# Kernel optimization log

Hardware: AMD Instinct MI355X
Metric: run time of the kernel (lower is better)

Reference implementation:

```python
import jax, jax.numpy as jnp
import numpy as np

B, L, D, H, S = 2, 2048, 1024, 16, 4
Dh = D // H
EPS = 1e-5


def setup_inputs() -> dict:
    key = jax.random.key(0)
    ks = jax.random.split(key, 12)
    sc = 0.02
    w = lambda k, shape: (jax.random.normal(k, shape, jnp.float32) * sc)
    M = 2 * S  # number of MHA blocks / dense linears
    inp = {
        "response": jax.random.normal(ks[0], (B, L, D), jnp.float32),
        "mask": jnp.broadcast_to(jnp.tril(jnp.ones((L, L), bool)), (B, L, L)),
        "Wq": w(ks[1], (M, D, D)), "bq": w(ks[2], (M, D)),
        "Wk": w(ks[3], (M, D, D)), "bk": w(ks[4], (M, D)),
        "Wv": w(ks[5], (M, D, D)), "bv": w(ks[6], (M, D)),
        "Wo": w(ks[7], (M, D, D)), "bo": w(ks[8], (M, D)),
        "Wd": w(ks[9], (M, D, D)), "bd": w(ks[10], (M, D)),
    }
    return inp


def _ln(x):
    # fresh LayerNorm(d) with default weight=1, bias=0, eps=1e-5
    m = jnp.mean(x, axis=-1, keepdims=True)
    v = jnp.mean((x - m) ** 2, axis=-1, keepdims=True)
    return (x - m) * jax.lax.rsqrt(v + EPS)


def _linear(x, W, b):
    # torch Linear: x @ W.T + b
    return jnp.einsum('bld,od->blo', x, W) + b


def _mha(x, i, mask, Wq, bq, Wk, bk, Wv, bv, Wo, bo):
    # self-attention: q = k = v = x
    split = lambda y: y.reshape(B, L, H, Dh).transpose(0, 2, 1, 3)  # (B,H,L,Dh)
    q = split(_linear(x, Wq[i], bq[i]))
    k = split(_linear(x, Wk[i], bk[i]))
    v = split(_linear(x, Wv[i], bv[i]))
    scores = jnp.einsum('bhqd,bhkd->bhqk', q, k) / jnp.sqrt(jnp.float32(Dh))
    if mask is not None:
        scores = jnp.where(mask[:, None, :, :], scores, -jnp.inf)
    p = jnp.nan_to_num(jax.nn.softmax(scores, axis=-1))
    o = jnp.einsum('bhqk,bhkd->bhqd', p, v).transpose(0, 2, 1, 3).reshape(B, L, D)
    return _linear(o, Wo[i], bo[i])


def reference(response, mask, Wq, bq, Wk, bk, Wv, bv, Wo, bo, Wd, bd):
    x = response
    for i in range(S):
        # masked self-attention + residual + LN
        x = _ln(x + _mha(x, 2 * i, mask, Wq, bq, Wk, bk, Wv, bv, Wo, bo))
        # encoder-attention sublayer (encMem is None -> unmasked self-attention)
        x = _ln(x + _mha(x, 2 * i + 1, None, Wq, bq, Wk, bk, Wv, bv, Wo, bo))
        # dense: linear[2i](LeakyReLU(linear[2i+1](x)))
        h = jax.nn.leaky_relu(_linear(x, Wd[2 * i + 1], bd[2 * i + 1]), negative_slope=0.01)
        h = _linear(h, Wd[2 * i], bd[2 * i])
        x = _ln(x + h)
    return x
```

## Files before the change

kernel.cpp:

```cpp
#include <hip/hip_runtime.h>
#include <stdint.h>
#include <stddef.h>

typedef __attribute__((ext_vector_type(8))) _Float16 f16x8;
typedef __attribute__((ext_vector_type(4))) _Float16 f16x4;
typedef __attribute__((ext_vector_type(4))) float    f32x4;

#define NB 2
#define NL 2048
#define ND 1024
#define NH 16
#define NROWS (NB*NL)

__device__ __forceinline__ void async16(void* lds, const void* g) {
  __builtin_amdgcn_global_load_lds(
      (const __attribute__((address_space(1))) void*)g,
      (__attribute__((address_space(3))) void*)lds, 16, 0, 0);
}

struct CvtArgs { const float* in[5]; _Float16* out[5]; };

__global__ __launch_bounds__(256) void cvt_all(CvtArgs a, int n4)
{
  const float* in  = a.in[blockIdx.z];
  _Float16*   out  = a.out[blockIdx.z];
  for (int i = blockIdx.x * blockDim.x + threadIdx.x; i < n4;
       i += gridDim.x * blockDim.x) {
    float4 v = ((const float4*)in)[i];
    f16x4 o = {(_Float16)v.x, (_Float16)v.y, (_Float16)v.z, (_Float16)v.w};
    ((f16x4*)out)[i] = o;
  }
}

__global__ __launch_bounds__(256) void init_x(
    const float* __restrict__ r, float* __restrict__ x,
    _Float16* __restrict__ xh, int n4)
{
  for (int i = blockIdx.x * blockDim.x + threadIdx.x; i < n4;
       i += gridDim.x * blockDim.x) {
    float4 v = ((const float4*)r)[i];
    ((float4*)x)[i] = v;
    f16x4 o = {(_Float16)v.x, (_Float16)v.y, (_Float16)v.z, (_Float16)v.w};
    ((f16x4*)xh)[i] = o;
  }
}

struct GArgs {
  const _Float16* A;
  const _Float16* B[3];
  const float*    bias[3];
  void*           out[3];
  int             mode[3];
  int             ksplit;
};

__global__ __launch_bounds__(256, 2) void gemm_bt(GArgs ga)
{
  __shared__ _Float16 As[2][128 * 64];
  __shared__ _Float16 Bs[2][128 * 64];
  const int tid = threadIdx.x;
  const int w = tid >> 6, l = tid & 63;
  const int ql = l & 15, g = l >> 4;
  const int z = blockIdx.z;
  const int widx = ga.ksplit ? 0 : (blockIdx.x >> 3);
  const _Float16* Bw  = ga.B[widx];
  const float*   bias = ga.bias[widx];
  void*          outp = ga.ksplit ? ga.out[z] : ga.out[widx];
  const int      mode = ga.mode[widx];
  const int kbeg = ga.ksplit ? z * (ND / 2) : 0;
  const int kend = ga.ksplit ? kbeg + ND / 2 : ND;
  const bool dobias = (!ga.ksplit) || (z == 0);
  const int brow = blockIdx.y * 128;
  const int bcol = (blockIdx.x & 7) * 128;
  const int wm = w >> 1, wn = w & 1;
  f32x4 acc[4][4] = {};

  const int srow = w * 32 + (l >> 3);
  const int scol = ((l & 7) ^ (l >> 3)) << 3;
  const _Float16* Ag = ga.A + (size_t)(brow + srow) * ND + scol;
  const _Float16* Bg = Bw   + (size_t)(bcol + srow) * ND + scol;

#define STAGE(buf, k0_)                                                  \
  {                                                                      \
    _Float16* AsW = &As[buf][w * 2048];                                  \
    _Float16* BsW = &Bs[buf][w * 2048];                                  \
    _Pragma("unroll")                                                    \
    for (int i = 0; i < 4; ++i) {                                        \
      async16(AsW + i * 512, Ag + (size_t)i * 8 * ND + (k0_));           \
      async16(BsW + i * 512, Bg + (size_t)i * 8 * ND + (k0_));           \
    }                                                                    \
  }

  STAGE(0, kbeg);
  for (int k0 = kbeg; k0 < kend; k0 += 64) {
    const int cur = ((k0 - kbeg) >> 6) & 1;
    if (k0 + 64 < kend) {
      STAGE(cur ^ 1, k0 + 64);
      asm volatile("s_waitcnt vmcnt(8)" ::: "memory");
    } else {
      asm volatile("s_waitcnt vmcnt(0)" ::: "memory");
    }
    __builtin_amdgcn_s_barrier();
#pragma unroll
    for (int ks = 0; ks < 64; ks += 32) {
      const int cx = (ks + g * 8) ^ ((ql & 7) << 3);
      f16x8 af[4], bf[4];
#pragma unroll
      for (int mi = 0; mi < 4; ++mi)
        af[mi] = *(const f16x8*)&As[cur][(wm * 64 + mi * 16 + ql) * 64 + cx];
#pragma unroll
      for (int nj = 0; nj < 4; ++nj)
        bf[nj] = *(const f16x8*)&Bs[cur][(wn * 64 + nj * 16 + ql) * 64 + cx];
#pragma unroll
      for (int mi = 0; mi < 4; ++mi)
#pragma unroll
        for (int nj = 0; nj < 4; ++nj)
          acc[mi][nj] = __builtin_amdgcn_mfma_f32_16x16x32_f16(
              af[mi], bf[nj], acc[mi][nj], 0, 0, 0);
    }
    asm volatile("s_waitcnt lgkmcnt(0)" ::: "memory");
    __builtin_amdgcn_s_barrier();
  }
#undef STAGE

  const int colb = bcol + wn * 64;
  const int rowb = brow + wm * 64 + g * 4;
  if (mode == 3) {
    _Float16* vt = (_Float16*)outp;
    const int bb = rowb >> 11;
#pragma unroll
    for (int nj = 0; nj < 4; ++nj) {
      const int col = colb + nj * 16 + ql;
      const float bv = bias[col];
      const int hh = col >> 6, d = col & 63;
      _Float16* vrow = vt + ((size_t)((bb * NH + hh) * 64 + d)) * NL;
#pragma unroll
      for (int mi = 0; mi < 4; ++mi) {
        const int krow = (rowb + mi * 16) & (NL - 1);
        f16x4 o;
#pragma unroll
        for (int r = 0; r < 4; ++r) o[r] = (_Float16)(acc[mi][nj][r] + bv);
        *(f16x4*)(vrow + krow) = o;
      }
    }
  } else {
    _Float16* oh = (_Float16*)outp;
#pragma unroll
    for (int nj = 0; nj < 4; ++nj) {
      const int col = colb + nj * 16 + ql;
      const float bv = dobias ? bias[col] : 0.f;
#pragma unroll
      for (int mi = 0; mi < 4; ++mi) {
#pragma unroll
        for (int r = 0; r < 4; ++r) {
          float v = acc[mi][nj][r] + bv;
          if (mode == 2) v = v > 0.f ? v : 0.01f * v;
          oh[(size_t)(rowb + mi * 16 + r) * ND + col] = (_Float16)v;
        }
      }
    }
  }
}

template<bool CAUSAL>
__global__ __launch_bounds__(512, 4) void attn_fwd(
    const _Float16* __restrict__ Q, const _Float16* __restrict__ K,
    const _Float16* __restrict__ Vt, _Float16* __restrict__ O)
{
  __shared__ _Float16 kv[3][2][64 * 64];
  __shared__ unsigned int pls[8][8 * 34];
  const int tid = threadIdx.x;
  const int w = tid >> 6, l = tid & 63;
  const int ql = l & 15, g = l >> 4;
  const int h = blockIdx.y, b = blockIdx.z;
  const int qt = (CAUSAL && b) ? (NL / 128 - 1 - (int)blockIdx.x) : blockIdx.x;
  const int qrow = qt * 128 + w * 16 + ql;

  const _Float16* Qp = Q + (size_t)(b * NL + qrow) * ND + h * 64 + g * 8;
  const f16x8 bq0 = *(const f16x8*)Qp;
  const f16x8 bq1 = *(const f16x8*)(Qp + 32);

  const int srow = w * 8 + (l >> 3);
  const int scol = ((l & 7) ^ (l >> 3)) << 3;
  const _Float16* Kg = K  + ((size_t)(b * NL) + srow) * ND + h * 64 + scol;
  const _Float16* Vg = Vt + ((size_t)((b * NH + h) * 64 + srow)) * NL + scol;

  const int msk  = (ql & 7) << 3;
  const int offA = ql * 64 + ((     g * 8) ^ msk);
  const int offB = ql * 64 + ((32 + g * 8) ^ msk);

  unsigned int* pw = &pls[w][0];
  f32x4 ot[4] = {};
  float s_run = 0.f;
  const int ntiles = CAUSAL ? (qt * 2 + 2) : (NL / 64);
  const float SCL = 0.125f * 1.44269504089f;
  const float M2  = 4.0f * 1.44269504089f;

  async16(&kv[0][0][w * 512], Kg);
  async16(&kv[0][1][w * 512], Vg);

  int cbuf = 0, sbuf = 1;
  for (int kt = 0; kt < ntiles; ++kt) {
    const size_t nk0 = (size_t)((kt + 1 < ntiles) ? kt + 1 : kt) * 64;
    async16(&kv[sbuf][0][w * 512], Kg + nk0 * ND);
    async16(&kv[sbuf][1][w * 512], Vg + nk0);
    asm volatile("s_waitcnt vmcnt(2)" ::: "memory");
    __builtin_amdgcn_s_barrier();

    const _Float16* kb = &kv[cbuf][0][0];
    const _Float16* vb = &kv[cbuf][1][0];
    const int k0 = kt * 64;
    f32x4 st[4] = {};
#pragma unroll
    for (int sub = 0; sub < 4; ++sub) {
      const f16x8 a0 = *(const f16x8*)&kb[sub * 1024 + offA];
      const f16x8 a1 = *(const f16x8*)&kb[sub * 1024 + offB];
      st[sub] = __builtin_amdgcn_mfma_f32_16x16x32_f16(a0, bq0, st[sub], 0, 0, 0);
      st[sub] = __builtin_amdgcn_mfma_f32_16x16x32_f16(a1, bq1, st[sub], 0, 0, 0);
    }
    float ps = 0.f;
    float pv[16];
#pragma unroll
    for (int sub = 0; sub < 4; ++sub)
#pragma unroll
      for (int r = 0; r < 4; ++r) {
        float p = exp2f(__builtin_fmaf(st[sub][r], SCL, -M2));
        if (CAUSAL && (k0 + sub * 16 + g * 4 + r) > qrow) p = 0.f;
        pv[sub * 4 + r] = p;
        ps += p;
      }
    ps += __shfl_xor(ps, 16);
    ps += __shfl_xor(ps, 32);
    s_run += ps;

#pragma unroll
    for (int sub = 0; sub < 2; ++sub) {
      uint2 uu;
      uu.x = __builtin_bit_cast(unsigned int,
                __builtin_amdgcn_cvt_pkrtz(pv[sub * 4 + 0], pv[sub * 4 + 1]));
      uu.y = __builtin_bit_cast(unsigned int,
                __builtin_amdgcn_cvt_pkrtz(pv[sub * 4 + 2], pv[sub * 4 + 3]));
      *(uint2*)&pw[(sub * 4 + g) * 34 + 2 * ql] = uu;
    }
    {
      uint2 lo = *(const uint2*)&pw[(2 * g    ) * 34 + 2 * ql];
      uint2 hi = *(const uint2*)&pw[(2 * g + 1) * 34 + 2 * ql];
      uint4 ui; ui.x = lo.x; ui.y = lo.y; ui.z = hi.x; ui.w = hi.y;
      const f16x8 pf = __builtin_bit_cast(f16x8, ui);
#pragma unroll
      for (int dt = 0; dt < 4; ++dt) {
        const f16x8 vf = *(const f16x8*)&vb[dt * 1024 + offA];
        ot[dt] = __builtin_amdgcn_mfma_f32_16x16x32_f16(vf, pf, ot[dt], 0, 0, 0);
      }
    }
#pragma unroll
    for (int sub = 2; sub < 4; ++sub) {
      uint2 uu;
      uu.x = __builtin_bit_cast(unsigned int,
                __builtin_amdgcn_cvt_pkrtz(pv[sub * 4 + 0], pv[sub * 4 + 1]));
      uu.y = __builtin_bit_cast(unsigned int,
                __builtin_amdgcn_cvt_pkrtz(pv[sub * 4 + 2], pv[sub * 4 + 3]));
      *(uint2*)&pw[((sub - 2) * 4 + g) * 34 + 2 * ql] = uu;
    }
    {
      uint2 lo = *(const uint2*)&pw[(2 * g    ) * 34 + 2 * ql];
      uint2 hi = *(const uint2*)&pw[(2 * g + 1) * 34 + 2 * ql];
      uint4 ui; ui.x = lo.x; ui.y = lo.y; ui.z = hi.x; ui.w = hi.y;
      const f16x8 pf = __builtin_bit_cast(f16x8, ui);
#pragma unroll
      for (int dt = 0; dt < 4; ++dt) {
        const f16x8 vf = *(const f16x8*)&vb[dt * 1024 + offB];
        ot[dt] = __builtin_amdgcn_mfma_f32_16x16x32_f16(vf, pf, ot[dt], 0, 0, 0);
      }
    }
    cbuf = sbuf;
    sbuf = sbuf + 1 == 3 ? 0 : sbuf + 1;
  }

  const float inv = 1.f / s_run;
#pragma unroll
  for (int dt = 0; dt < 4; ++dt) {
    f16x4 o;
#pragma unroll
    for (int r = 0; r < 4; ++r) o[r] = (_Float16)(ot[dt][r] * inv);
    *(f16x4*)(O + (size_t)(b * NL + qrow) * ND + h * 64 + dt * 16 + g * 4) = o;
  }
}

__global__ __launch_bounds__(256) void resid_ln(
    const float* __restrict__ x, const _Float16* __restrict__ d0,
    const _Float16* __restrict__ d1,
    float* __restrict__ xo, _Float16* __restrict__ xh)
{
  const int row = blockIdx.x, tid = threadIdx.x;
  const float4 xv = ((const float4*)(x + (size_t)row * ND))[tid];
  const f16x4 v0 = ((const f16x4*)(d0 + (size_t)row * ND))[tid];
  const f16x4 v1 = ((const f16x4*)(d1 + (size_t)row * ND))[tid];
  const float a = xv.x + (float)v0[0] + (float)v1[0];
  const float b = xv.y + (float)v0[1] + (float)v1[1];
  const float c = xv.z + (float)v0[2] + (float)v1[2];
  const float d = xv.w + (float)v0[3] + (float)v1[3];
  float s = a + b + c + d;
  float ss = a * a + b * b + c * c + d * d;
#pragma unroll
  for (int m = 1; m < 64; m <<= 1) {
    s  += __shfl_xor(s, m);
    ss += __shfl_xor(ss, m);
  }
  __shared__ float red[8];
  if ((tid & 63) == 0) { red[tid >> 6] = s; red[4 + (tid >> 6)] = ss; }
  __syncthreads();
  const float S  = red[0] + red[1] + red[2] + red[3];
  const float SS = red[4] + red[5] + red[6] + red[7];
  const float mean = S * (1.0f / ND);
  const float var  = SS * (1.0f / ND) - mean * mean;
  const float rstd = rsqrtf(fmaxf(var, 0.f) + 1e-5f);
  float4 y;
  y.x = (a - mean) * rstd; y.y = (b - mean) * rstd;
  y.z = (c - mean) * rstd; y.w = (d - mean) * rstd;
  ((float4*)(xo + (size_t)row * ND))[tid] = y;
  f16x4 yh = {(_Float16)y.x, (_Float16)y.y, (_Float16)y.z, (_Float16)y.w};
  ((f16x4*)(xh + (size_t)row * ND))[tid] = yh;
}

extern "C" void kernel_launch(void* const* d_in, const int* in_sizes, int n_in,
                              void* d_out, int out_size, void* d_ws, size_t ws_size,
                              hipStream_t stream)
{
  (void)in_sizes; (void)n_in; (void)out_size; (void)ws_size;
  const float* response = (const float*)d_in[0];
  const float* Wq = (const float*)d_in[2];
  const float* bq = (const float*)d_in[3];
  const float* Wk = (const float*)d_in[4];
  const float* bk = (const float*)d_in[5];
  const float* Wv = (const float*)d_in[6];
  const float* bv = (const float*)d_in[7];
  const float* Wo = (const float*)d_in[8];
  const float* bo = (const float*)d_in[9];
  const float* Wd = (const float*)d_in[10];
  const float* bd = (const float*)d_in[11];
  float* x = (float*)d_out;

  const size_t MB = 1024 * 1024;
  char* p = (char*)d_ws;
  _Float16* Wq_h = (_Float16*)(p + 0 * MB);
  _Float16* Wk_h = (_Float16*)(p + 16 * MB);
  _Float16* Wv_h = (_Float16*)(p + 32 * MB);
  _Float16* Wo_h = (_Float16*)(p + 48 * MB);
  _Float16* Wd_h = (_Float16*)(p + 64 * MB);
  _Float16* xh   = (_Float16*)(p + 80 * MB);
  _Float16* Qh   = (_Float16*)(p + 88 * MB);
  _Float16* Kh   = (_Float16*)(p + 96 * MB);
  _Float16* Vth  = (_Float16*)(p + 104 * MB);
  _Float16* Oh   = (_Float16*)(p + 112 * MB);
  _Float16* h1   = Qh;
  _Float16* t0   = (_Float16*)(p + 96 * MB);
  _Float16* t1   = (_Float16*)(p + 104 * MB);

  const int wn4 = 8 * 1024 * 1024 / 4;
  CvtArgs ca = { { Wq, Wk, Wv, Wo, Wd }, { Wq_h, Wk_h, Wv_h, Wo_h, Wd_h } };
  cvt_all<<<dim3(256, 1, 5), 256, 0, stream>>>(ca, wn4);
  init_x<<<1024, 256, 0, stream>>>(response, x, xh, NROWS * ND / 4);

  const dim3 g3(24, NROWS / 128, 1);
  const dim3 gs(8, NROWS / 128, 2);
  const dim3 gf(8, NROWS / 128, 1);
  const dim3 agrid(NL / 128, NH, NB);

  for (int i = 0; i < 4; ++i) {
    for (int sub = 0; sub < 2; ++sub) {
      const int m = 2 * i + sub;
      const size_t wo = (size_t)m * MB;
      const size_t bf = (size_t)m * 1024;
      GArgs qkv = { xh,
                    { Wq_h + wo, Wk_h + wo, Wv_h + wo },
                    { bq + bf, bk + bf, bv + bf },
                    { Qh, Kh, Vth }, { 0, 0, 3 }, 0 };
      gemm_bt<<<g3, 256, 0, stream>>>(qkv);
      if (sub == 0) attn_fwd<true ><<<agrid, 512, 0, stream>>>(Qh, Kh, Vth, Oh);
      else          attn_fwd<false><<<agrid, 512, 0, stream>>>(Qh, Kh, Vth, Oh);
      GArgs oprj = { Oh,
                     { Wo_h + wo, nullptr, nullptr },
                     { bo + bf, nullptr, nullptr },
                     { t0, t1, nullptr }, { 0, 0, 0 }, 1 };
      gemm_bt<<<gs, 256, 0, stream>>>(oprj);
      resid_ln<<<NROWS, 256, 0, stream>>>(x, t0, t1, x, xh);
    }
    const size_t w1 = (size_t)(2 * i + 1) * MB, b1 = (size_t)(2 * i + 1) * 1024;
    const size_t w0 = (size_t)(2 * i) * MB,     b0 = (size_t)(2 * i) * 1024;
    GArgs f1 = { xh,
                 { Wd_h + w1, nullptr, nullptr },
                 { bd + b1, nullptr, nullptr },
                 { h1, nullptr, nullptr }, { 2, 0, 0 }, 0 };
    gemm_bt<<<gf, 256, 0, stream>>>(f1);
    GArgs f2 = { h1,
                 { Wd_h + w0, nullptr, nullptr },
                 { bd + b0, nullptr, nullptr },
                 { t0, t1, nullptr }, { 0, 0, 0 }, 1 };
    gemm_bt<<<gs, 256, 0, stream>>>(f2);
    resid_ln<<<NROWS, 256, 0, stream>>>(x, t0, t1, x, xh);
  }
}
```

Before: 1.237 ms.

## Keep residual stream in fp16, widen conversion stores, raise MFMA wave priority

Drops the fp32 copy of the residual stream: each residual+LayerNorm reads and writes only the fp16 activations, and fp32 output is written only in the final layer. The weight and input conversion kernels now emit 8-wide fp16 stores, and the weight conversion grid is larger. s_setprio is raised around the MFMA blocks in the GEMM and attention loops so matrix-heavy waves are favoured by the scheduler. The residual path loses precision by accumulating in fp16 across twelve sublayers.

```diff
diff --git a/kernel.cpp b/kernel.cpp
--- a/kernel.cpp
+++ b/kernel.cpp
@@ -20,28 +20,30 @@
 
 struct CvtArgs { const float* in[5]; _Float16* out[5]; };
 
-__global__ __launch_bounds__(256) void cvt_all(CvtArgs a, int n4)
+__global__ __launch_bounds__(256) void cvt_all(CvtArgs a, int n8)
 {
   const float* in  = a.in[blockIdx.z];
   _Float16*   out  = a.out[blockIdx.z];
-  for (int i = blockIdx.x * blockDim.x + threadIdx.x; i < n4;
+  for (int i = blockIdx.x * blockDim.x + threadIdx.x; i < n8;
        i += gridDim.x * blockDim.x) {
-    float4 v = ((const float4*)in)[i];
-    f16x4 o = {(_Float16)v.x, (_Float16)v.y, (_Float16)v.z, (_Float16)v.w};
-    ((f16x4*)out)[i] = o;
+    float4 v0 = ((const float4*)in)[2 * i];
+    float4 v1 = ((const float4*)in)[2 * i + 1];
+    f16x8 o = {(_Float16)v0.x, (_Float16)v0.y, (_Float16)v0.z, (_Float16)v0.w,
+               (_Float16)v1.x, (_Float16)v1.y, (_Float16)v1.z, (_Float16)v1.w};
+    ((f16x8*)out)[i] = o;
   }
 }
 
 __global__ __launch_bounds__(256) void init_x(
-    const float* __restrict__ r, float* __restrict__ x,
-    _Float16* __restrict__ xh, int n4)
-{
-  for (int i = blockIdx.x * blockDim.x + threadIdx.x; i < n4;
+    const float* __restrict__ r, _Float16* __restrict__ xh, int n8)
+{
+  for (int i = blockIdx.x * blockDim.x + threadIdx.x; i < n8;
        i += gridDim.x * blockDim.x) {
-    float4 v = ((const float4*)r)[i];
-    ((float4*)x)[i] = v;
-    f16x4 o = {(_Float16)v.x, (_Float16)v.y, (_Float16)v.z, (_Float16)v.w};
-    ((f16x4*)xh)[i] = o;
+    float4 v0 = ((const float4*)r)[2 * i];
+    float4 v1 = ((const float4*)r)[2 * i + 1];
+    f16x8 o = {(_Float16)v0.x, (_Float16)v0.y, (_Float16)v0.z, (_Float16)v0.w,
+               (_Float16)v1.x, (_Float16)v1.y, (_Float16)v1.z, (_Float16)v1.w};
+    ((f16x8*)xh)[i] = o;
   }
 }
 
@@ -101,6 +103,7 @@
       asm volatile("s_waitcnt vmcnt(0)" ::: "memory");
     }
     __builtin_amdgcn_s_barrier();
+    __builtin_amdgcn_s_setprio(1);
 #pragma unroll
     for (int ks = 0; ks < 64; ks += 32) {
       const int cx = (ks + g * 8) ^ ((ql & 7) << 3);
@@ -118,6 +121,7 @@
           acc[mi][nj] = __builtin_amdgcn_mfma_f32_16x16x32_f16(
               af[mi], bf[nj], acc[mi][nj], 0, 0, 0);
     }
+    __builtin_amdgcn_s_setprio(0);
     asm volatile("s_waitcnt lgkmcnt(0)" ::: "memory");
     __builtin_amdgcn_s_barrier();
   }
@@ -211,6 +215,7 @@
     const _Float16* vb = &kv[cbuf][1][0];
     const int k0 = kt * 64;
     f32x4 st[4] = {};
+    __builtin_amdgcn_s_setprio(1);
 #pragma unroll
     for (int sub = 0; sub < 4; ++sub) {
       const f16x8 a0 = *(const f16x8*)&kb[sub * 1024 + offA];
@@ -218,6 +223,7 @@
       st[sub] = __builtin_amdgcn_mfma_f32_16x16x32_f16(a0, bq0, st[sub], 0, 0, 0);
       st[sub] = __builtin_amdgcn_mfma_f32_16x16x32_f16(a1, bq1, st[sub], 0, 0, 0);
     }
+    __builtin_amdgcn_s_setprio(0);
     float ps = 0.f;
     float pv[16];
 #pragma unroll
@@ -247,11 +253,13 @@
       uint2 hi = *(const uint2*)&pw[(2 * g + 1) * 34 + 2 * ql];
       uint4 ui; ui.x = lo.x; ui.y = lo.y; ui.z = hi.x; ui.w = hi.y;
       const f16x8 pf = __builtin_bit_cast(f16x8, ui);
+      __builtin_amdgcn_s_setprio(1);
 #pragma unroll
       for (int dt = 0; dt < 4; ++dt) {
         const f16x8 vf = *(const f16x8*)&vb[dt * 1024 + offA];
         ot[dt] = __builtin_amdgcn_mfma_f32_16x16x32_f16(vf, pf, ot[dt], 0, 0, 0);
       }
+      __builtin_amdgcn_s_setprio(0);
     }
 #pragma unroll
     for (int sub = 2; sub < 4; ++sub) {
@@ -267,11 +275,13 @@
       uint2 hi = *(const uint2*)&pw[(2 * g + 1) * 34 + 2 * ql];
       uint4 ui; ui.x = lo.x; ui.y = lo.y; ui.z = hi.x; ui.w = hi.y;
       const f16x8 pf = __builtin_bit_cast(f16x8, ui);
+      __builtin_amdgcn_s_setprio(1);
 #pragma unroll
       for (int dt = 0; dt < 4; ++dt) {
         const f16x8 vf = *(const f16x8*)&vb[dt * 1024 + offB];
         ot[dt] = __builtin_amdgcn_mfma_f32_16x16x32_f16(vf, pf, ot[dt], 0, 0, 0);
       }
+      __builtin_amdgcn_s_setprio(0);
     }
     cbuf = sbuf;
     sbuf = sbuf + 1 == 3 ? 0 : sbuf + 1;
@@ -287,19 +297,20 @@
   }
 }
 
+template<bool FINAL>
 __global__ __launch_bounds__(256) void resid_ln(
-    const float* __restrict__ x, const _Float16* __restrict__ d0,
+    const _Float16* __restrict__ xh_in, const _Float16* __restrict__ d0,
     const _Float16* __restrict__ d1,
-    float* __restrict__ xo, _Float16* __restrict__ xh)
+    _Float16* __restrict__ xh_out, float* __restrict__ xf)
 {
   const int row = blockIdx.x, tid = threadIdx.x;
-  const float4 xv = ((const float4*)(x + (size_t)row * ND))[tid];
+  const f16x4 xv = ((const f16x4*)(xh_in + (size_t)row * ND))[tid];
   const f16x4 v0 = ((const f16x4*)(d0 + (size_t)row * ND))[tid];
   const f16x4 v1 = ((const f16x4*)(d1 + (size_t)row * ND))[tid];
-  const float a = xv.x + (float)v0[0] + (float)v1[0];
-  const float b = xv.y + (float)v0[1] + (float)v1[1];
-  const float c = xv.z + (float)v0[2] + (float)v1[2];
-  const float d = xv.w + (float)v0[3] + (float)v1[3];
+  const float a = (float)xv[0] + (float)v0[0] + (float)v1[0];
+  const float b = (float)xv[1] + (float)v0[1] + (float)v1[1];
+  const float c = (float)xv[2] + (float)v0[2] + (float)v1[2];
+  const float d = (float)xv[3] + (float)v0[3] + (float)v1[3];
   float s = a + b + c + d;
   float ss = a * a + b * b + c * c + d * d;
 #pragma unroll
@@ -315,12 +326,15 @@
   const float mean = S * (1.0f / ND);
   const float var  = SS * (1.0f / ND) - mean * mean;
   const float rstd = rsqrtf(fmaxf(var, 0.f) + 1e-5f);
-  float4 y;
-  y.x = (a - mean) * rstd; y.y = (b - mean) * rstd;
-  y.z = (c - mean) * rstd; y.w = (d - mean) * rstd;
-  ((float4*)(xo + (size_t)row * ND))[tid] = y;
-  f16x4 yh = {(_Float16)y.x, (_Float16)y.y, (_Float16)y.z, (_Float16)y.w};
-  ((f16x4*)(xh + (size_t)row * ND))[tid] = yh;
+  const float ya = (a - mean) * rstd, yb = (b - mean) * rstd;
+  const float yc = (c - mean) * rstd, yd = (d - mean) * rstd;
+  if (FINAL) {
+    float4 y; y.x = ya; y.y = yb; y.z = yc; y.w = yd;
+    ((float4*)(xf + (size_t)row * ND))[tid] = y;
+  } else {
+    f16x4 yh = {(_Float16)ya, (_Float16)yb, (_Float16)yc, (_Float16)yd};
+    ((f16x4*)(xh_out + (size_t)row * ND))[tid] = yh;
+  }
 }
 
 extern "C" void kernel_launch(void* const* d_in, const int* in_sizes, int n_in,
@@ -339,7 +353,7 @@
   const float* bo = (const float*)d_in[9];
   const float* Wd = (const float*)d_in[10];
   const float* bd = (const float*)d_in[11];
-  float* x = (float*)d_out;
+  float* xf = (float*)d_out;
 
   const size_t MB = 1024 * 1024;
   char* p = (char*)d_ws;
@@ -357,10 +371,10 @@
   _Float16* t0   = (_Float16*)(p + 96 * MB);
   _Float16* t1   = (_Float16*)(p + 104 * MB);
 
-  const int wn4 = 8 * 1024 * 1024 / 4;
+  const int wn8 = 8 * 1024 * 1024 / 8;
   CvtArgs ca = { { Wq, Wk, Wv, Wo, Wd }, { Wq_h, Wk_h, Wv_h, Wo_h, Wd_h } };
-  cvt_all<<<dim3(256, 1, 5), 256, 0, stream>>>(ca, wn4);
-  init_x<<<1024, 256, 0, stream>>>(response, x, xh, NROWS * ND / 4);
+  cvt_all<<<dim3(512, 1, 5), 256, 0, stream>>>(ca, wn8);
+  init_x<<<1024, 256, 0, stream>>>(response, xh, NROWS * ND / 8);
 
   const dim3 g3(24, NROWS / 128, 1);
   const dim3 gs(8, NROWS / 128, 2);
@@ -384,7 +398,7 @@
                      { bo + bf, nullptr, nullptr },
                      { t0, t1, nullptr }, { 0, 0, 0 }, 1 };
       gemm_bt<<<gs, 256, 0, stream>>>(oprj);
-      resid_ln<<<NROWS, 256, 0, stream>>>(x, t0, t1, x, xh);
+      resid_ln<false><<<NROWS, 256, 0, stream>>>(xh, t0, t1, xh, nullptr);
     }
     const size_t w1 = (size_t)(2 * i + 1) * MB, b1 = (size_t)(2 * i + 1) * 1024;
     const size_t w0 = (size_t)(2 * i) * MB,     b0 = (size_t)(2 * i) * 1024;
@@ -398,6 +412,7 @@
                  { bd + b0, nullptr, nullptr },
                  { t0, t1, nullptr }, { 0, 0, 0 }, 1 };
     gemm_bt<<<gs, 256, 0, stream>>>(f2);
-    resid_ln<<<NROWS, 256, 0, stream>>>(x, t0, t1, x, xh);
-  }
-}
+    if (i == 3) resid_ln<true ><<<NROWS, 256, 0, stream>>>(xh, t0, t1, nullptr, xf);
+    else        resid_ln<false><<<NROWS, 256, 0, stream>>>(xh, t0, t1, xh, nullptr);
+  }
+}
```

Measured after the change: 1.194 ms. -3.5%, faster.
